# Performance work log

Hardware: AMD Instinct MI355X
Metric: run time of the kernel (lower is better)

## Reference

```python
import jax, jax.numpy as jnp
import numpy as np

B, T, C = 8, 2048, 1024
HEAD = 64

def setup_inputs() -> dict:
    key = jax.random.key(0)
    k1, k2 = jax.random.split(key)
    x = jax.random.normal(k1, (B, T, C), dtype=jnp.float32)
    W_qkv = jax.random.normal(k2, (C, 3 * HEAD), dtype=jnp.float32) * (C ** -0.5)
    return {"x": x, "W_qkv": W_qkv}

def reference(x, W_qkv):
    # qkv projection (bias-free Linear): [B,T,3*HEAD]
    qkv = x @ W_qkv
    q, k, v = jnp.split(qkv, 3, axis=-1)  # each [B,T,HEAD]
    # scaled dot-product scores [B,T,T]
    dots = jnp.einsum('btd,bsd->bts', q, k) * (HEAD ** -0.5)
    # causal mask (tril == keep)
    Tq = x.shape[1]
    causal = jnp.tril(jnp.ones((Tq, Tq), dtype=bool))
    dots = jnp.where(causal, dots, -jnp.inf)
    attn = jax.nn.softmax(dots, axis=-1)
    # dropout p=0.0 (eval) -> identity
    out = jnp.einsum('bts,bsd->btd', attn, v)  # [B,T,HEAD]
    return out
```

## Files before the change

### kernel.cpp

```cpp
#include <hip/hip_runtime.h>
#include <stdint.h>

#define NB 8
#define NT 2048
#define NC 1024
#define HD 64

typedef __attribute__((ext_vector_type(8)))  short s16x8;
typedef __attribute__((ext_vector_type(4)))  float f32x4;
typedef __attribute__((ext_vector_type(16))) float f32x16;

__device__ inline ushort f2b(float f) {
    union { float f; uint32_t u; } c; c.f = f;
    uint32_t u = c.u;
    uint32_t r = (u + 0x7fffu + ((u >> 16) & 1u)) >> 16;
    return (ushort)r;
}

__device__ inline uint32_t cvt_pk_bf16(float lo, float hi) {
    uint32_t r;
    asm("v_cvt_pk_bf16_f32 %0, %1, %2" : "=v"(r) : "v"(lo), "v"(hi));
    return r;
}

__device__ inline void gload_lds16(const void* gsrc, void* lds) {
    __builtin_amdgcn_global_load_lds(
        (const __attribute__((address_space(1))) void*)gsrc,
        (__attribute__((address_space(3))) void*)lds, 16, 0, 0);
}

__global__ __launch_bounds__(256) void wprep(const float* __restrict__ W,
                                             ushort* __restrict__ wt) {
    int tid = blockIdx.x * 256 + threadIdx.x;
    int n = tid >> 10;
    int k = tid & 1023;
    float v = W[k * 192 + n];
    if (n < 64) v *= 0.125f * 1.4426950408889634f;
    wt[n * 1024 + k] = f2b(v);
}

__global__ __launch_bounds__(512, 1) void qkv_gemm(const float* __restrict__ x,
                                                   const ushort* __restrict__ wt,
                                                   ushort* __restrict__ qs,
                                                   ushort* __restrict__ kk,
                                                   ushort* __restrict__ vt) {
    __shared__ __align__(16) char Al[3][16384];
    __shared__ __align__(16) char Wl[3][24576];

    const int tid = threadIdx.x;
    const int wv  = tid >> 6;
    const int ls  = tid & 63;
    const int r16 = ls & 15;
    const int hi4 = ls >> 4;
    const int g   = wv >> 2;
    const int c   = wv & 3;
    const int row0 = blockIdx.x * 64;

    const int srow = ls >> 3;
    const int sslt = (ls & 7) ^ srow;
    const float* xA = x + (size_t)(row0 + wv * 8 + srow) * NC + sslt * 4;
    const ushort* wS0 = wt + (size_t)(wv * 24 + 0  + srow) * 1024 + sslt * 8;
    const ushort* wS1 = wt + (size_t)(wv * 24 + 8  + srow) * 1024 + sslt * 8;
    const ushort* wS2 = wt + (size_t)(wv * 24 + 16 + srow) * 1024 + sslt * 8;

    const int key = r16 & 7;
    int aoff[2];
#pragma unroll
    for (int m = 0; m < 2; ++m)
        aoff[m] = (g * 32 + m * 16 + r16) * 128 + (((hi4 * 2) ^ key) << 4);
    int bnrow[3];
#pragma unroll
    for (int nf = 0; nf < 3; ++nf)
        bnrow[nf] = (c * 48 + nf * 16 + r16) * 128;
    int bkey[2];
#pragma unroll
    for (int kq = 0; kq < 2; ++kq)
        bkey[kq] = ((kq * 4 + hi4) ^ key) << 4;

    f32x4 acc[2][3];
#pragma unroll
    for (int i = 0; i < 2; ++i)
#pragma unroll
        for (int j = 0; j < 3; ++j)
#pragma unroll
            for (int e = 0; e < 4; ++e) acc[i][j][e] = 0.f;

    auto STAGE = [&](int t) {
        int bb = t % 3;
        gload_lds16(xA + t * 64,      &Al[bb][0 * 8192 + wv * 1024]);
        gload_lds16(xA + t * 64 + 32, &Al[bb][1 * 8192 + wv * 1024]);
        gload_lds16(wS0 + t * 64, &Wl[bb][(wv * 24 + 0) * 128]);
        gload_lds16(wS1 + t * 64, &Wl[bb][(wv * 24 + 8) * 128]);
        gload_lds16(wS2 + t * 64, &Wl[bb][(wv * 24 + 16) * 128]);
    };

    auto COMPUTE = [&](int bb) {
#pragma unroll
        for (int kq = 0; kq < 2; ++kq) {
            s16x8 af[2], bf[3];
#pragma unroll
            for (int m = 0; m < 2; ++m) {
                const char* base = &Al[bb][kq * 8192];
                float4 a0 = *(const float4*)(base + aoff[m]);
                float4 a1 = *(const float4*)(base + (aoff[m] ^ 16));
                union { uint32_t w[4]; s16x8 v; } pk;
                pk.w[0] = cvt_pk_bf16(a0.x, a0.y);
                pk.w[1] = cvt_pk_bf16(a0.z, a0.w);
                pk.w[2] = cvt_pk_bf16(a1.x, a1.y);
                pk.w[3] = cvt_pk_bf16(a1.z, a1.w);
                af[m] = pk.v;
            }
#pragma unroll
            for (int nf = 0; nf < 3; ++nf)
                bf[nf] = *(const s16x8*)(&Wl[bb][0] + bnrow[nf] + bkey[kq]);
#pragma unroll
            for (int m = 0; m < 2; ++m)
#pragma unroll
                for (int nf = 0; nf < 3; ++nf)
                    acc[m][nf] = __builtin_amdgcn_mfma_f32_16x16x32_bf16(
                        af[m], bf[nf], acc[m][nf], 0, 0, 0);
        }
    };

    STAGE(0); STAGE(1);

    for (int t = 0; t < 14; ++t) {
        asm volatile("s_waitcnt vmcnt(5)" ::: "memory");
        __builtin_amdgcn_s_barrier();
        STAGE(t + 2);
        COMPUTE(t % 3);
    }
    asm volatile("s_waitcnt vmcnt(5)" ::: "memory");
    __builtin_amdgcn_s_barrier();
    COMPUTE(14 % 3);
    asm volatile("s_waitcnt vmcnt(0)" ::: "memory");
    __builtin_amdgcn_s_barrier();
    COMPUTE(15 % 3);

    const int b = row0 >> 11;
#pragma unroll
    for (int m = 0; m < 2; ++m) {
        const int rbase = row0 + g * 32 + m * 16 + hi4 * 4;
#pragma unroll
        for (int nf = 0; nf < 3; ++nf) {
            int colg = c * 48 + nf * 16 + r16;
            f32x4 v = acc[m][nf];
            if (colg < 64) {
#pragma unroll
                for (int j = 0; j < 4; ++j)
                    qs[(size_t)(rbase + j) * HD + colg] = f2b(v[j]);
            } else if (colg < 128) {
#pragma unroll
                for (int j = 0; j < 4; ++j)
                    kk[(size_t)(rbase + j) * HD + (colg - 64)] = f2b(v[j]);
            } else {
                int d = colg - 128;
                union { ushort4 s; ushort u[4]; } pk;
#pragma unroll
                for (int j = 0; j < 4; ++j) pk.u[j] = f2b(v[j]);
                *(ushort4*)(&vt[((size_t)(b * 64 + d)) * NT + (rbase & (NT - 1))]) = pk.s;
            }
        }
    }
}

__global__ __launch_bounds__(256) void attn(const ushort* __restrict__ qs,
                                            const ushort* __restrict__ kk,
                                            const ushort* __restrict__ vt,
                                            float* __restrict__ out) {
    __shared__ float ob[4][64][33];
    __shared__ float ml[4][2][32];

    const int bid  = blockIdx.x;
    const int b    = bid & 7;
    const int tile = 63 - (bid >> 3);
    const int tid  = threadIdx.x;
    const int wv   = tid >> 6;
    const int l    = tid & 63;
    const int qcol = l & 31;
    const int hi   = l >> 5;
    const int r0   = tile * 32;

    const ushort* qb = qs + ((size_t)(b * NT + r0)) * HD;
    const ushort* kb = kk + (size_t)b * NT * HD;
    const ushort* vb = vt + (size_t)b * HD * NT;

    s16x8 qf[4];
#pragma unroll
    for (int c = 0; c < 4; ++c)
        qf[c] = *(const s16x8*)(qb + (size_t)qcol * HD + c * 16 + hi * 8);

    f32x16 o0, o1;
#pragma unroll
    for (int i = 0; i < 16; ++i) { o0[i] = 0.f; o1[i] = 0.f; }
    float m = -3.0e30f, lsum = 0.f;

    if (wv <= tile) {
        s16x8 kf[4], vf[4];
        {
            const ushort* kr = kb + (size_t)(wv * 32 + qcol) * HD;
#pragma unroll
            for (int c = 0; c < 4; ++c)
                kf[c] = *(const s16x8*)(kr + c * 16 + hi * 8);
#pragma unroll
            for (int dt = 0; dt < 2; ++dt)
#pragma unroll
                for (int kc = 0; kc < 2; ++kc)
                    vf[dt * 2 + kc] = *(const s16x8*)(vb + (size_t)(dt * 32 + qcol) * NT
                                                      + wv * 32 + kc * 16 + hi * 8);
        }

        for (int kt = wv; kt <= tile; kt += 4) {
            f32x16 s;
#pragma unroll
            for (int i = 0; i < 16; ++i) s[i] = 0.f;
#pragma unroll
            for (int c = 0; c < 4; ++c)
                s = __builtin_amdgcn_mfma_f32_32x32x16_bf16(kf[c], qf[c], s, 0, 0, 0);

            s16x8 kfn[4], vfn[4];
            const bool more = (kt + 4 <= tile);
            if (more) {
                const ushort* kr = kb + (size_t)((kt + 4) * 32 + qcol) * HD;
#pragma unroll
                for (int c = 0; c < 4; ++c)
                    kfn[c] = *(const s16x8*)(kr + c * 16 + hi * 8);
#pragma unroll
                for (int dt = 0; dt < 2; ++dt)
#pragma unroll
                    for (int kc = 0; kc < 2; ++kc)
                        vfn[dt * 2 + kc] = *(const s16x8*)(vb + (size_t)(dt * 32 + qcol) * NT
                                                           + (kt + 4) * 32 + kc * 16 + hi * 8);
            }

            const bool diag = (kt == tile);
            float p[16];
#pragma unroll
            for (int r = 0; r < 16; ++r) {
                int klocal = (r & 3) + 8 * (r >> 2) + 4 * hi;
                float sv = s[r];
                if (diag && klocal > qcol) sv = -3.0e30f;
                p[r] = sv;
            }
            float pmax = p[0];
#pragma unroll
            for (int r = 1; r < 16; ++r) pmax = fmaxf(pmax, p[r]);
            pmax = fmaxf(pmax, __shfl_xor(pmax, 32));
            float mnew = fmaxf(m, pmax);
            float corr = exp2f(m - mnew);
            m = mnew;
            float rs = 0.f;
#pragma unroll
            for (int r = 0; r < 16; ++r) { p[r] = exp2f(p[r] - mnew); rs += p[r]; }
            rs += __shfl_xor(rs, 32);
            lsum = lsum * corr + rs;
#pragma unroll
            for (int i = 0; i < 16; ++i) { o0[i] *= corr; o1[i] *= corr; }

#pragma unroll
            for (int kc = 0; kc < 2; ++kc) {
                int pb = kc * 8;
                uint32_t a0 = cvt_pk_bf16(p[pb + 0], p[pb + 1]);
                uint32_t a1 = cvt_pk_bf16(p[pb + 2], p[pb + 3]);
                uint32_t b0 = cvt_pk_bf16(p[pb + 4], p[pb + 5]);
                uint32_t b1 = cvt_pk_bf16(p[pb + 6], p[pb + 7]);
                uint32_t a0x = __shfl_xor(a0, 32);
                uint32_t a1x = __shfl_xor(a1, 32);
                uint32_t b0x = __shfl_xor(b0, 32);
                uint32_t b1x = __shfl_xor(b1, 32);
                union { uint32_t w[4]; s16x8 v; } frag;
                frag.w[0] = hi ? b0x : a0;
                frag.w[1] = hi ? b1x : a1;
                frag.w[2] = hi ? b0  : a0x;
                frag.w[3] = hi ? b1  : a1x;
                o0 = __builtin_amdgcn_mfma_f32_32x32x16_bf16(vf[0 * 2 + kc], frag.v, o0, 0, 0, 0);
                o1 = __builtin_amdgcn_mfma_f32_32x32x16_bf16(vf[1 * 2 + kc], frag.v, o1, 0, 0, 0);
            }

            if (more) {
#pragma unroll
                for (int c = 0; c < 4; ++c) kf[c] = kfn[c];
#pragma unroll
                for (int c = 0; c < 4; ++c) vf[c] = vfn[c];
            }
        }
    }

#pragma unroll
    for (int r = 0; r < 16; ++r) {
        int d = (r & 3) + 8 * (r >> 2) + 4 * hi;
        ob[wv][d][qcol]      = o0[r];
        ob[wv][d + 32][qcol] = o1[r];
    }
    if (hi == 0) {
        ml[wv][0][qcol] = m;
        ml[wv][1][qcol] = lsum;
    }
    __syncthreads();

    const int q  = tid >> 3;
    const int j0 = (tid & 7) * 8;
    float mw[4];
#pragma unroll
    for (int w = 0; w < 4; ++w) mw[w] = ml[w][0][q];
    float M = fmaxf(fmaxf(mw[0], mw[1]), fmaxf(mw[2], mw[3]));
    float sw[4]; float L = 0.f;
#pragma unroll
    for (int w = 0; w < 4; ++w) {
        sw[w] = exp2f(mw[w] - M);
        L += sw[w] * ml[w][1][q];
    }
    float invL = 1.0f / L;
    float vals[8];
#pragma unroll
    for (int j = 0; j < 8; ++j) {
        int d = j0 + j;
        float acc = 0.f;
#pragma unroll
        for (int w = 0; w < 4; ++w) acc += sw[w] * ob[w][d][q];
        vals[j] = acc * invL;
    }
    float* orow = out + ((size_t)(b * NT + r0 + q)) * HD + j0;
    *(float4*)(orow)     = make_float4(vals[0], vals[1], vals[2], vals[3]);
    *(float4*)(orow + 4) = make_float4(vals[4], vals[5], vals[6], vals[7]);
}

extern "C" void kernel_launch(void* const* d_in, const int* in_sizes, int n_in,
                              void* d_out, int out_size, void* d_ws, size_t ws_size,
                              hipStream_t stream) {
    const float* x = (const float*)d_in[0];
    const float* W = (const float*)d_in[1];
    float* out = (float*)d_out;

    ushort* qs = (ushort*)d_ws;
    ushort* kk = qs + (size_t)NB * NT * HD;
    ushort* vt = kk + (size_t)NB * NT * HD;
    ushort* wt = vt + (size_t)NB * NT * HD;

    wprep<<<768, 256, 0, stream>>>(W, wt);
    qkv_gemm<<<256, 512, 0, stream>>>(x, wt, qs, kk, vt);
    attn<<<512, 256, 0, stream>>>(qs, kk, vt, out);
}
```

Measured before the change: 57.05 us.

## Keep QKV weight slice resident in LDS and stream x directly into registers

The QKV projection kernel is re-tiled so each block owns 256 rows and one 48-column group of the output. That group's full bf16 weight slice is loaded into LDS once at the start, replacing the triple-buffered LDS pipeline that restaged both x and W tiles every K step. x is now read straight from global memory into registers with a two-step register prefetch. This removes per-step barriers and the LDS staging of activations. In exchange, each x row is fetched by four separate blocks, which may sit on different XCDs, and the 128KB LDS footprint limits occupancy to one block per CU.

```diff
diff --git a/kernel.cpp b/kernel.cpp
--- a/kernel.cpp
+++ b/kernel.cpp
@@ -39,43 +39,52 @@
     wt[n * 1024 + k] = f2b(v);
 }
 
-__global__ __launch_bounds__(512, 1) void qkv_gemm(const float* __restrict__ x,
+__global__ __launch_bounds__(512, 2) void qkv_gemm(const float* __restrict__ x,
                                                    const ushort* __restrict__ wt,
                                                    ushort* __restrict__ qs,
                                                    ushort* __restrict__ kk,
                                                    ushort* __restrict__ vt) {
-    __shared__ __align__(16) char Al[3][16384];
-    __shared__ __align__(16) char Wl[3][24576];
+    __shared__ __align__(16) char Wl[131072];
 
     const int tid = threadIdx.x;
     const int wv  = tid >> 6;
     const int ls  = tid & 63;
     const int r16 = ls & 15;
     const int hi4 = ls >> 4;
-    const int g   = wv >> 2;
-    const int c   = wv & 3;
-    const int row0 = blockIdx.x * 64;
-
-    const int srow = ls >> 3;
-    const int sslt = (ls & 7) ^ srow;
-    const float* xA = x + (size_t)(row0 + wv * 8 + srow) * NC + sslt * 4;
-    const ushort* wS0 = wt + (size_t)(wv * 24 + 0  + srow) * 1024 + sslt * 8;
-    const ushort* wS1 = wt + (size_t)(wv * 24 + 8  + srow) * 1024 + sslt * 8;
-    const ushort* wS2 = wt + (size_t)(wv * 24 + 16 + srow) * 1024 + sslt * 8;
-
-    const int key = r16 & 7;
-    int aoff[2];
-#pragma unroll
-    for (int m = 0; m < 2; ++m)
-        aoff[m] = (g * 32 + m * 16 + r16) * 128 + (((hi4 * 2) ^ key) << 4);
-    int bnrow[3];
-#pragma unroll
-    for (int nf = 0; nf < 3; ++nf)
-        bnrow[nf] = (c * 48 + nf * 16 + r16) * 128;
-    int bkey[2];
-#pragma unroll
-    for (int kq = 0; kq < 2; ++kq)
-        bkey[kq] = ((kq * 4 + hi4) ^ key) << 4;
+    const int bid = blockIdx.x;
+    const int cg  = bid & 3;
+    const int row0 = (bid >> 2) * 256;
+
+    {
+        int nsrc = cg * 48 + ls;
+        if (nsrc > 191) nsrc = 191;
+        const ushort* wsrc = wt + (size_t)nsrc * 1024;
+#pragma unroll
+        for (int j = 0; j < 16; ++j) {
+            int k8 = wv * 16 + j;
+            gload_lds16(wsrc + k8 * 8, &Wl[k8 * 1024]);
+        }
+    }
+
+    const float* pA0 = x + (size_t)(row0 + wv * 32 + 0  + r16) * NC + hi4 * 8;
+    const float* pA1 = x + (size_t)(row0 + wv * 32 + 16 + r16) * NC + hi4 * 8;
+
+    float4 ab[2][2][2][2];
+
+#define LOADA(S, T)                                                          \
+    do {                                                                     \
+        _Pragma("unroll")                                                    \
+        for (int kq_ = 0; kq_ < 2; ++kq_) {                                  \
+            _Pragma("unroll")                                                \
+            for (int h_ = 0; h_ < 2; ++h_) {                                 \
+                ab[S][0][kq_][h_] = *(const float4*)(pA0 + (T) * 64 + kq_ * 32 + h_ * 4); \
+                ab[S][1][kq_][h_] = *(const float4*)(pA1 + (T) * 64 + kq_ * 32 + h_ * 4); \
+            }                                                                \
+        }                                                                    \
+    } while (0)
+
+    LOADA(0, 0);
+    LOADA(1, 1);
 
     f32x4 acc[2][3];
 #pragma unroll
@@ -85,65 +94,52 @@
 #pragma unroll
             for (int e = 0; e < 4; ++e) acc[i][j][e] = 0.f;
 
-    auto STAGE = [&](int t) {
-        int bb = t % 3;
-        gload_lds16(xA + t * 64,      &Al[bb][0 * 8192 + wv * 1024]);
-        gload_lds16(xA + t * 64 + 32, &Al[bb][1 * 8192 + wv * 1024]);
-        gload_lds16(wS0 + t * 64, &Wl[bb][(wv * 24 + 0) * 128]);
-        gload_lds16(wS1 + t * 64, &Wl[bb][(wv * 24 + 8) * 128]);
-        gload_lds16(wS2 + t * 64, &Wl[bb][(wv * 24 + 16) * 128]);
-    };
-
-    auto COMPUTE = [&](int bb) {
-#pragma unroll
-        for (int kq = 0; kq < 2; ++kq) {
-            s16x8 af[2], bf[3];
-#pragma unroll
-            for (int m = 0; m < 2; ++m) {
-                const char* base = &Al[bb][kq * 8192];
-                float4 a0 = *(const float4*)(base + aoff[m]);
-                float4 a1 = *(const float4*)(base + (aoff[m] ^ 16));
+    asm volatile("s_waitcnt vmcnt(0)" ::: "memory");
+    __builtin_amdgcn_s_barrier();
+
+#pragma unroll
+    for (int t = 0; t < 16; ++t) {
+        const int set = t & 1;
+        s16x8 af[2][2];
+#pragma unroll
+        for (int m = 0; m < 2; ++m)
+#pragma unroll
+            for (int kq = 0; kq < 2; ++kq) {
+                float4 a0 = ab[set][m][kq][0];
+                float4 a1 = ab[set][m][kq][1];
                 union { uint32_t w[4]; s16x8 v; } pk;
                 pk.w[0] = cvt_pk_bf16(a0.x, a0.y);
                 pk.w[1] = cvt_pk_bf16(a0.z, a0.w);
                 pk.w[2] = cvt_pk_bf16(a1.x, a1.y);
                 pk.w[3] = cvt_pk_bf16(a1.z, a1.w);
-                af[m] = pk.v;
-            }
+                af[m][kq] = pk.v;
+            }
+        if (t + 2 < 16) LOADA(set, t + 2);
+        __builtin_amdgcn_sched_barrier(0);
+#pragma unroll
+        for (int kq = 0; kq < 2; ++kq) {
+            const int k8 = t * 8 + kq * 4 + hi4;
+            s16x8 bf[3];
 #pragma unroll
             for (int nf = 0; nf < 3; ++nf)
-                bf[nf] = *(const s16x8*)(&Wl[bb][0] + bnrow[nf] + bkey[kq]);
+                bf[nf] = *(const s16x8*)(&Wl[k8 * 1024 + (nf * 16 + r16) * 16]);
 #pragma unroll
             for (int m = 0; m < 2; ++m)
 #pragma unroll
                 for (int nf = 0; nf < 3; ++nf)
                     acc[m][nf] = __builtin_amdgcn_mfma_f32_16x16x32_bf16(
-                        af[m], bf[nf], acc[m][nf], 0, 0, 0);
-        }
-    };
-
-    STAGE(0); STAGE(1);
-
-    for (int t = 0; t < 14; ++t) {
-        asm volatile("s_waitcnt vmcnt(5)" ::: "memory");
-        __builtin_amdgcn_s_barrier();
-        STAGE(t + 2);
-        COMPUTE(t % 3);
-    }
-    asm volatile("s_waitcnt vmcnt(5)" ::: "memory");
-    __builtin_amdgcn_s_barrier();
-    COMPUTE(14 % 3);
-    asm volatile("s_waitcnt vmcnt(0)" ::: "memory");
-    __builtin_amdgcn_s_barrier();
-    COMPUTE(15 % 3);
+                        af[m][kq], bf[nf], acc[m][nf], 0, 0, 0);
+        }
+    }
+#undef LOADA
 
     const int b = row0 >> 11;
 #pragma unroll
     for (int m = 0; m < 2; ++m) {
-        const int rbase = row0 + g * 32 + m * 16 + hi4 * 4;
+        const int rbase = row0 + wv * 32 + m * 16 + hi4 * 4;
 #pragma unroll
         for (int nf = 0; nf < 3; ++nf) {
-            int colg = c * 48 + nf * 16 + r16;
+            int colg = cg * 48 + nf * 16 + r16;
             f32x4 v = acc[m][nf];
             if (colg < 64) {
 #pragma unroll
```

Measured after the change: 79.97 us. 1.4x slower.

## Split QKV GEMM columns across two blocks with double-buffered smaller tiles

Applied to the files above, without the earlier changes.

The QKV projection GEMM now launches 512 blocks of 256 threads, each computing 64 rows by 96 output columns instead of 64 by 192. The LDS staging changes from a triple buffer to a double buffer with a full drain after each step, and the launch bounds change so two blocks can share a CU. This is meant to raise the number of blocks in flight (256 blocks previously covered the CUs only about once) and to cut LDS use per block. The cost is that every x row tile is read twice from global memory, and the pipeline is shallower, with a full vmcnt(0) wait on each iteration.

```diff
diff --git a/kernel.cpp b/kernel.cpp
--- a/kernel.cpp
+++ b/kernel.cpp
@@ -39,127 +39,123 @@
     wt[n * 1024 + k] = f2b(v);
 }
 
-__global__ __launch_bounds__(512, 1) void qkv_gemm(const float* __restrict__ x,
+__global__ __launch_bounds__(256, 2) void qkv_gemm(const float* __restrict__ x,
                                                    const ushort* __restrict__ wt,
                                                    ushort* __restrict__ qs,
                                                    ushort* __restrict__ kk,
                                                    ushort* __restrict__ vt) {
-    __shared__ __align__(16) char Al[3][16384];
-    __shared__ __align__(16) char Wl[3][24576];
+    __shared__ __align__(16) char Al[2][16384];
+    __shared__ __align__(16) char Wl[2][12288];
 
     const int tid = threadIdx.x;
     const int wv  = tid >> 6;
     const int ls  = tid & 63;
     const int r16 = ls & 15;
     const int hi4 = ls >> 4;
-    const int g   = wv >> 2;
-    const int c   = wv & 3;
-    const int row0 = blockIdx.x * 64;
-
-    const int srow = ls >> 3;
-    const int sslt = (ls & 7) ^ srow;
-    const float* xA = x + (size_t)(row0 + wv * 8 + srow) * NC + sslt * 4;
-    const ushort* wS0 = wt + (size_t)(wv * 24 + 0  + srow) * 1024 + sslt * 8;
-    const ushort* wS1 = wt + (size_t)(wv * 24 + 8  + srow) * 1024 + sslt * 8;
-    const ushort* wS2 = wt + (size_t)(wv * 24 + 16 + srow) * 1024 + sslt * 8;
+    const int bid = blockIdx.x;
+    const int rowtile = bid & 255;
+    const int cg  = bid >> 8;
+    const int row0 = rowtile * 64;
+
+    const float* xsrc[4];
+#pragma unroll
+    for (int j = 0; j < 4; ++j) {
+        int r = wv * 16 + j * 4 + (ls >> 4);
+        int slot = (ls & 15) ^ (r & 7);
+        xsrc[j] = x + (size_t)(row0 + r) * NC + slot * 4;
+    }
+    const ushort* wsrc[3];
+#pragma unroll
+    for (int j = 0; j < 3; ++j) {
+        int n = wv * 24 + j * 8 + (ls >> 3);
+        int slot = (ls & 7) ^ (n & 7);
+        wsrc[j] = wt + (size_t)(cg * 96 + n) * 1024 + slot * 8;
+    }
 
     const int key = r16 & 7;
+    const int arow = wv * 16 + r16;
     int aoff[2];
 #pragma unroll
-    for (int m = 0; m < 2; ++m)
-        aoff[m] = (g * 32 + m * 16 + r16) * 128 + (((hi4 * 2) ^ key) << 4);
-    int bnrow[3];
-#pragma unroll
-    for (int nf = 0; nf < 3; ++nf)
-        bnrow[nf] = (c * 48 + nf * 16 + r16) * 128;
+    for (int kq = 0; kq < 2; ++kq)
+        aoff[kq] = arow * 256 + (((kq * 8 + hi4 * 2) ^ key) << 4);
+    int bnrow[6];
+#pragma unroll
+    for (int nf = 0; nf < 6; ++nf)
+        bnrow[nf] = (nf * 16 + r16) * 128;
     int bkey[2];
 #pragma unroll
     for (int kq = 0; kq < 2; ++kq)
-        bkey[kq] = ((kq * 4 + hi4) ^ key) << 4;
-
-    f32x4 acc[2][3];
-#pragma unroll
-    for (int i = 0; i < 2; ++i)
+        bkey[kq] = (((kq * 4 + hi4) ^ key) << 4);
+
+    f32x4 acc[6];
+#pragma unroll
+    for (int j = 0; j < 6; ++j)
+#pragma unroll
+        for (int e = 0; e < 4; ++e) acc[j][e] = 0.f;
+
+    auto STAGE = [&](int t) {
+        int bb = t & 1;
+#pragma unroll
+        for (int j = 0; j < 4; ++j)
+            gload_lds16(xsrc[j] + t * 64, &Al[bb][wv * 4096 + j * 1024]);
 #pragma unroll
         for (int j = 0; j < 3; ++j)
-#pragma unroll
-            for (int e = 0; e < 4; ++e) acc[i][j][e] = 0.f;
-
-    auto STAGE = [&](int t) {
-        int bb = t % 3;
-        gload_lds16(xA + t * 64,      &Al[bb][0 * 8192 + wv * 1024]);
-        gload_lds16(xA + t * 64 + 32, &Al[bb][1 * 8192 + wv * 1024]);
-        gload_lds16(wS0 + t * 64, &Wl[bb][(wv * 24 + 0) * 128]);
-        gload_lds16(wS1 + t * 64, &Wl[bb][(wv * 24 + 8) * 128]);
-        gload_lds16(wS2 + t * 64, &Wl[bb][(wv * 24 + 16) * 128]);
+            gload_lds16(wsrc[j] + t * 64, &Wl[bb][wv * 3072 + j * 1024]);
     };
 
     auto COMPUTE = [&](int bb) {
 #pragma unroll
         for (int kq = 0; kq < 2; ++kq) {
-            s16x8 af[2], bf[3];
-#pragma unroll
-            for (int m = 0; m < 2; ++m) {
-                const char* base = &Al[bb][kq * 8192];
-                float4 a0 = *(const float4*)(base + aoff[m]);
-                float4 a1 = *(const float4*)(base + (aoff[m] ^ 16));
-                union { uint32_t w[4]; s16x8 v; } pk;
-                pk.w[0] = cvt_pk_bf16(a0.x, a0.y);
-                pk.w[1] = cvt_pk_bf16(a0.z, a0.w);
-                pk.w[2] = cvt_pk_bf16(a1.x, a1.y);
-                pk.w[3] = cvt_pk_bf16(a1.z, a1.w);
-                af[m] = pk.v;
-            }
-#pragma unroll
-            for (int nf = 0; nf < 3; ++nf)
+            float4 a0 = *(const float4*)(&Al[bb][0] + aoff[kq]);
+            float4 a1 = *(const float4*)(&Al[bb][0] + (aoff[kq] ^ 16));
+            union { uint32_t w[4]; s16x8 v; } pk;
+            pk.w[0] = cvt_pk_bf16(a0.x, a0.y);
+            pk.w[1] = cvt_pk_bf16(a0.z, a0.w);
+            pk.w[2] = cvt_pk_bf16(a1.x, a1.y);
+            pk.w[3] = cvt_pk_bf16(a1.z, a1.w);
+            s16x8 af = pk.v;
+            s16x8 bf[6];
+#pragma unroll
+            for (int nf = 0; nf < 6; ++nf)
                 bf[nf] = *(const s16x8*)(&Wl[bb][0] + bnrow[nf] + bkey[kq]);
 #pragma unroll
-            for (int m = 0; m < 2; ++m)
-#pragma unroll
-                for (int nf = 0; nf < 3; ++nf)
-                    acc[m][nf] = __builtin_amdgcn_mfma_f32_16x16x32_bf16(
-                        af[m], bf[nf], acc[m][nf], 0, 0, 0);
+            for (int nf = 0; nf < 6; ++nf)
+                acc[nf] = __builtin_amdgcn_mfma_f32_16x16x32_bf16(
+                    af, bf[nf], acc[nf], 0, 0, 0);
         }
     };
 
-    STAGE(0); STAGE(1);
-
-    for (int t = 0; t < 14; ++t) {
-        asm volatile("s_waitcnt vmcnt(5)" ::: "memory");
-        __builtin_amdgcn_s_barrier();
-        STAGE(t + 2);
-        COMPUTE(t % 3);
-    }
-    asm volatile("s_waitcnt vmcnt(5)" ::: "memory");
-    __builtin_amdgcn_s_barrier();
-    COMPUTE(14 % 3);
+    STAGE(0);
     asm volatile("s_waitcnt vmcnt(0)" ::: "memory");
     __builtin_amdgcn_s_barrier();
-    COMPUTE(15 % 3);
+
+    for (int t = 0; t < 16; ++t) {
+        if (t < 15) STAGE(t + 1);
+        COMPUTE(t & 1);
+        asm volatile("s_waitcnt vmcnt(0)" ::: "memory");
+        __builtin_amdgcn_s_barrier();
+    }
 
     const int b = row0 >> 11;
-#pragma unroll
-    for (int m = 0; m < 2; ++m) {
-        const int rbase = row0 + g * 32 + m * 16 + hi4 * 4;
-#pragma unroll
-        for (int nf = 0; nf < 3; ++nf) {
-            int colg = c * 48 + nf * 16 + r16;
-            f32x4 v = acc[m][nf];
-            if (colg < 64) {
-#pragma unroll
-                for (int j = 0; j < 4; ++j)
-                    qs[(size_t)(rbase + j) * HD + colg] = f2b(v[j]);
-            } else if (colg < 128) {
-#pragma unroll
-                for (int j = 0; j < 4; ++j)
-                    kk[(size_t)(rbase + j) * HD + (colg - 64)] = f2b(v[j]);
-            } else {
-                int d = colg - 128;
-                union { ushort4 s; ushort u[4]; } pk;
-#pragma unroll
-                for (int j = 0; j < 4; ++j) pk.u[j] = f2b(v[j]);
-                *(ushort4*)(&vt[((size_t)(b * 64 + d)) * NT + (rbase & (NT - 1))]) = pk.s;
-            }
+    const int rbase = row0 + wv * 16 + hi4 * 4;
+#pragma unroll
+    for (int nf = 0; nf < 6; ++nf) {
+        int colg = cg * 96 + nf * 16 + r16;
+        f32x4 v = acc[nf];
+        if (colg < 64) {
+#pragma unroll
+            for (int j = 0; j < 4; ++j)
+                qs[(size_t)(rbase + j) * HD + colg] = f2b(v[j]);
+        } else if (colg < 128) {
+#pragma unroll
+            for (int j = 0; j < 4; ++j)
+                kk[(size_t)(rbase + j) * HD + (colg - 64)] = f2b(v[j]);
+        } else {
+            int d = colg - 128;
+            union { ushort4 s; ushort u[4]; } pk;
+#pragma unroll
+            for (int j = 0; j < 4; ++j) pk.u[j] = f2b(v[j]);
+            *(ushort4*)(&vt[((size_t)(b * 64 + d)) * NT + (rbase & (NT - 1))]) = pk.s;
         }
     }
 }
@@ -338,6 +334,6 @@
     ushort* wt = vt + (size_t)NB * NT * HD;
 
     wprep<<<768, 256, 0, stream>>>(W, wt);
-    qkv_gemm<<<256, 512, 0, stream>>>(x, wt, qs, kk, vt);
+    qkv_gemm<<<512, 256, 0, stream>>>(x, wt, qs, kk, vt);
     attn<<<512, 256, 0, stream>>>(qs, kk, vt, out);
 }
```

After: 54.20 us. -5.0%, faster.
